# Performance work log

Measured on AMD Instinct MI355X. Metric: run time of the kernel, lower is better.

Reference implementation:

```python
import jax, jax.numpy as jnp
import numpy as np

B, L, D_LLM, C_OH, D = 256, 128, 1024, 64, 256
HEADS, LAYERS, EDGE_DIM, NET, E_PER = 4, 4, 64, 8, 256
N = B * L
DH = D // HEADS


def _layer_norm(x, g, b, eps=1e-5):
    m = x.mean(-1, keepdims=True)
    v = ((x - m) ** 2).mean(-1, keepdims=True)
    return (x - m) / jnp.sqrt(v + eps) * g + b


def _conv(h, src, dst, ea, Wq, bq, Wk, bk, Wv, bv, We, Ws, bs, Wb):
    # PyG TransformerConv (concat=True, beta=True, edge_dim): per-edge gather of Q(dst), K/V(src)
    q = (h @ Wq + bq)[dst].reshape(-1, HEADS, DH)
    k = (h @ Wk + bk)[src].reshape(-1, HEADS, DH)
    v = (h @ Wv + bv)[src].reshape(-1, HEADS, DH)
    e = (ea @ We).reshape(-1, HEADS, DH)
    k = k + e
    v = v + e
    alpha = (q * k).sum(-1) / jnp.sqrt(jnp.float32(DH))  # [E, H]
    amax = jax.ops.segment_max(alpha, dst, num_segments=N)  # segment softmax over dst
    ex = jnp.exp(alpha - amax[dst])
    den = jax.ops.segment_sum(ex, dst, num_segments=N)
    a = ex / den[dst]
    out = jax.ops.segment_sum(a[:, :, None] * v, dst, num_segments=N).reshape(N, D)
    xr = h @ Ws + bs  # root/skip projection
    beta = jax.nn.sigmoid(jnp.concatenate([out, xr, out - xr], axis=-1) @ Wb)  # [N,1]
    return beta * xr + (1.0 - beta) * out


def _gnorm(x, batch, w, b, ms, eps=1e-5):
    # PyG GraphNorm: per-graph mean with learnable mean_scale, per-graph variance
    cnt = jax.ops.segment_sum(jnp.ones((N,), x.dtype), batch, num_segments=B)[:, None]
    mean = jax.ops.segment_sum(x, batch, num_segments=B) / cnt
    out = x - mean[batch] * ms
    var = jax.ops.segment_sum(out * out, batch, num_segments=B) / cnt
    return w * out / jnp.sqrt(var + eps)[batch] + b


def _forward(atom_llm, atom_onehot, mask, edge_index, edge_type, batch,
             ln_llm_g, ln_llm_b, W_llm, b_llm, W_oh, edge_emb, edge_ln_g, edge_ln_b,
             Wq, bq, Wk, bk, Wv, bv, We, Ws, bs, Wb, gn_w, gn_b, gn_ms,
             W1, b1, W2, b2, out_ln_g, out_ln_b):
    x = (_layer_norm(atom_llm, ln_llm_g, ln_llm_b) @ W_llm + b_llm) + atom_onehot @ W_oh
    x = x * mask[..., None]
    h = x.reshape(N, D)  # all graphs full length L -> packing == reshape
    ea = _layer_norm(edge_emb[edge_type], edge_ln_g, edge_ln_b)
    src, dst = edge_index[0], edge_index[1]
    for l in range(LAYERS):
        h2 = _conv(h, src, dst, ea, Wq[l], bq[l], Wk[l], bk[l], Wv[l], bv[l], We[l], Ws[l], bs[l], Wb[l])
        h = _gnorm(h + h2, batch, gn_w[l], gn_b[l], gn_ms[l])
        h = jax.nn.gelu(h, approximate=False)
    ff = jax.nn.gelu(h @ W1 + b1, approximate=False) @ W2 + b2
    h = _layer_norm(h + ff, out_ln_g, out_ln_b)
    return h.reshape(B, L, D) * mask[..., None]


def setup_inputs():
    key = jax.random.key(0)
    ks = jax.random.split(key, 64)
    rng = np.random.default_rng(0)
    atom_llm = jax.random.normal(ks[0], (B, L, D_LLM), jnp.float32)
    atom_onehot = jax.random.uniform(ks[1], (B, L, C_OH), jnp.float32)
    mask = jnp.ones((B, L), jnp.float32)
    # per-graph random edges u != v, global offsets, undirected doubling
    u = rng.integers(0, L, size=(B, E_PER))
    v = (u + rng.integers(1, L, size=(B, E_PER))) % L
    et = rng.integers(0, NET, size=(B, E_PER)).reshape(-1)
    off = (np.arange(B) * L)[:, None]
    s = (u + off).reshape(-1)
    d = (v + off).reshape(-1)
    edge_index = jnp.asarray(np.stack([np.concatenate([s, d]), np.concatenate([d, s])]), jnp.int32)
    edge_type = jnp.asarray(np.concatenate([et, et]), jnp.int32)
    batch = jnp.repeat(jnp.arange(B, dtype=jnp.int32), L)

    def lin(k, i, o):
        s = 1.0 / np.sqrt(i)
        return jax.random.uniform(k, (i, o), jnp.float32, -s, s)

    st = lambda f, keys: jnp.stack([f(k) for k in keys])
    kq = jax.random.split(ks[10], LAYERS); kk = jax.random.split(ks[11], LAYERS)
    kv = jax.random.split(ks[12], LAYERS); ke = jax.random.split(ks[13], LAYERS)
    ksk = jax.random.split(ks[14], LAYERS); kb = jax.random.split(ks[15], LAYERS)
    return dict(
        atom_llm=atom_llm, atom_onehot=atom_onehot, mask=mask,
        edge_index=edge_index, edge_type=edge_type, batch=batch,
        ln_llm_g=jnp.ones((D_LLM,)), ln_llm_b=jnp.zeros((D_LLM,)),
        W_llm=lin(ks[2], D_LLM, D), b_llm=jnp.zeros((D,)),
        W_oh=lin(ks[3], C_OH, D),
        edge_emb=jax.random.normal(ks[4], (NET, EDGE_DIM), jnp.float32),
        edge_ln_g=jnp.ones((EDGE_DIM,)), edge_ln_b=jnp.zeros((EDGE_DIM,)),
        Wq=st(lambda k: lin(k, D, D), kq), bq=jnp.zeros((LAYERS, D)),
        Wk=st(lambda k: lin(k, D, D), kk), bk=jnp.zeros((LAYERS, D)),
        Wv=st(lambda k: lin(k, D, D), kv), bv=jnp.zeros((LAYERS, D)),
        We=st(lambda k: lin(k, EDGE_DIM, D), ke),
        Ws=st(lambda k: lin(k, D, D), ksk), bs=jnp.zeros((LAYERS, D)),
        Wb=st(lambda k: lin(k, 3 * D, 1), kb),
        gn_w=jnp.ones((LAYERS, D)), gn_b=jnp.zeros((LAYERS, D)), gn_ms=jnp.ones((LAYERS, D)),
        W1=lin(ks[6], D, 4 * D) * 0.5, b1=jnp.zeros((4 * D,)),
        W2=lin(ks[7], 4 * D, D) * 0.5, b2=jnp.zeros((D,)),
        out_ln_g=jnp.ones((D,)), out_ln_b=jnp.zeros((D,)),
    )


def reference(atom_llm, atom_onehot, mask, edge_index, edge_type, batch,
              ln_llm_g, ln_llm_b, W_llm, b_llm, W_oh, edge_emb, edge_ln_g, edge_ln_b,
              Wq, bq, Wk, bk, Wv, bv, We, Ws, bs, Wb, gn_w, gn_b, gn_ms,
              W1, b1, W2, b2, out_ln_g, out_ln_b):
    return _forward(atom_llm, atom_onehot, mask, edge_index, edge_type, batch,
                    ln_llm_g, ln_llm_b, W_llm, b_llm, W_oh, edge_emb, edge_ln_g, edge_ln_b,
                    Wq, bq, Wk, bk, Wv, bv, We, Ws, bs, Wb, gn_w, gn_b, gn_ms,
                    W1, b1, W2, b2, out_ln_g, out_ln_b)
```

## Files before the change

kernel.cpp:

```cpp
#include <hip/hip_runtime.h>
#include <math.h>

#define NB      256
#define LL      128
#define NN      32768
#define DLLM    1024
#define COH     64
#define DD      256
#define NLAYERS 4
#define EDIM    64
#define NETT    8
#define NE      131072

typedef unsigned short bf16_t;
typedef __bf16 bf16x8 __attribute__((ext_vector_type(8)));
typedef float f32x4v __attribute__((ext_vector_type(4)));

__device__ __forceinline__ float bf2f(bf16_t u){
    return __uint_as_float(((unsigned int)u) << 16);
}
__device__ __forceinline__ bf16_t f2bf(float f){
    unsigned int x = __float_as_uint(f);
    return (bf16_t)((x + 0x7fffu + ((x >> 16) & 1u)) >> 16);
}
__device__ __forceinline__ unsigned pack2(float a, float b){
    return (unsigned)f2bf(a) | ((unsigned)f2bf(b) << 16);
}
__device__ __forceinline__ float gelu_exact(float x){
    return 0.5f * x * (1.0f + erff(x * 0.70710678118654752440f));
}
__device__ __forceinline__ float wave_reduce_sum(float v){
#pragma unroll
    for (int off = 32; off; off >>= 1) v += __shfl_xor(v, off);
    return v;
}

__global__ void zero_kernel(int* __restrict__ p, int n){
    int i = blockIdx.x * blockDim.x + threadIdx.x;
    if (i < n) p[i] = 0;
}

__global__ __launch_bounds__(256)
void ln_concat_kernel(const float* __restrict__ A, const float* __restrict__ onehot,
                      const float* __restrict__ g, const float* __restrict__ b,
                      bf16_t* __restrict__ xln){
    int wave = threadIdx.x >> 6, lane = threadIdx.x & 63;
    int row = (blockIdx.x << 2) + wave;
    const float* p = A + (size_t)row * DLLM;
    float4 v[4];
    float s = 0.f, sq = 0.f;
#pragma unroll
    for (int c = 0; c < 4; c++){
        v[c] = *(const float4*)(p + c * 256 + (lane << 2));
        s  += v[c].x + v[c].y + v[c].z + v[c].w;
        sq += v[c].x*v[c].x + v[c].y*v[c].y + v[c].z*v[c].z + v[c].w*v[c].w;
    }
    s = wave_reduce_sum(s); sq = wave_reduce_sum(sq);
    float mean = s * (1.0f / DLLM);
    float var  = sq * (1.0f / DLLM) - mean * mean;
    float rstd = rsqrtf(var + 1e-5f);
    bf16_t* out = xln + (size_t)row * 1088;
#pragma unroll
    for (int c = 0; c < 4; c++){
        float4 g4 = *(const float4*)(g + c * 256 + (lane << 2));
        float4 b4 = *(const float4*)(b + c * 256 + (lane << 2));
        float rx = (v[c].x - mean) * rstd * g4.x + b4.x;
        float ry = (v[c].y - mean) * rstd * g4.y + b4.y;
        float rz = (v[c].z - mean) * rstd * g4.z + b4.z;
        float rw = (v[c].w - mean) * rstd * g4.w + b4.w;
        ushort4 u; u.x = f2bf(rx); u.y = f2bf(ry); u.z = f2bf(rz); u.w = f2bf(rw);
        *(ushort4*)(out + c * 256 + (lane << 2)) = u;
    }
    out[1024 + lane] = f2bf(onehot[(size_t)row * COH + lane]);
}

__global__ __launch_bounds__(256)
void edgeproj_kernel(const float* __restrict__ edge_emb,
                     const float* __restrict__ lg, const float* __restrict__ lb,
                     const float* __restrict__ We, float* __restrict__ eproj){
    int l = blockIdx.x >> 3, t = blockIdx.x & 7;
    __shared__ float ea[EDIM];
    int tid = threadIdx.x;
    if (tid < 64){
        float v = edge_emb[t * EDIM + tid];
        float s = v, sq = v * v;
#pragma unroll
        for (int off = 32; off; off >>= 1){ s += __shfl_xor(s, off); sq += __shfl_xor(sq, off); }
        float mean = s * (1.f/64.f);
        float var  = sq * (1.f/64.f) - mean * mean;
        float rstd = rsqrtf(var + 1e-5f);
        ea[tid] = (v - mean) * rstd * lg[tid] + lb[tid];
    }
    __syncthreads();
    const float* W = We + (size_t)l * EDIM * DD;
    float s = 0.f;
#pragma unroll
    for (int k = 0; k < EDIM; k++) s += ea[k] * W[k * DD + tid];
    eproj[((l << 3) + t) * DD + tid] = s;
}

__global__ void count_kernel(const int* __restrict__ dst, int* __restrict__ cnt){
    int e = blockIdx.x * blockDim.x + threadIdx.x;
    if (e < NE){
        int d = dst[e];
        if (d >= 0 && d < NN) atomicAdd(&cnt[d], 1);
    }
}

__global__ __launch_bounds__(1024)
void scan_kernel(const int* __restrict__ cnt, int* __restrict__ rowstart, int* __restrict__ cursor){
    __shared__ int sh[1024];
    int tid = threadIdx.x;
    int carry = 0;
    for (int base = 0; base < NN; base += 1024){
        int v = cnt[base + tid];
        sh[tid] = v; __syncthreads();
        for (int off = 1; off < 1024; off <<= 1){
            int t = (tid >= off) ? sh[tid - off] : 0;
            __syncthreads();
            sh[tid] += t;
            __syncthreads();
        }
        int excl = carry + sh[tid] - v;
        rowstart[base + tid] = excl;
        cursor[base + tid]   = excl;
        carry += sh[1023];
        __syncthreads();
    }
    if (tid == 0) rowstart[NN] = carry;
}

__global__ void scatter_kernel(const int* __restrict__ dst, int* __restrict__ cursor,
                               int* __restrict__ eidx){
    int e = blockIdx.x * blockDim.x + threadIdx.x;
    if (e < NE){
        int d = dst[e];
        if (d >= 0 && d < NN){
            int p = atomicAdd(&cursor[d], 1);
            if (p >= 0 && p < NE) eidx[p] = e;
        }
    }
}

__global__ void wcvt_in_kernel(const float* __restrict__ Wllm, const float* __restrict__ Woh,
                               bf16_t* __restrict__ dst){
    int idx = blockIdx.x * blockDim.x + threadIdx.x;
    if (idx >= 256 * 1088) return;
    int n = idx / 1088, k = idx % 1088;
    float v = (k < 1024) ? Wllm[(size_t)k * 256 + n] : Woh[(size_t)(k - 1024) * 256 + n];
    dst[idx] = f2bf(v);
}

__global__ void wcvt_qkvs_kernel(const float* __restrict__ Wq, const float* __restrict__ Wk,
                                 const float* __restrict__ Wv, const float* __restrict__ Ws,
                                 bf16_t* __restrict__ dst){
    int idx = blockIdx.x * blockDim.x + threadIdx.x;
    if (idx >= NLAYERS * 1024 * 256) return;
    int l = idx >> 18, rem = idx & 262143;
    int n = rem >> 8, k = rem & 255;
    int sel = n >> 8, nn = n & 255;
    const float* W = (sel == 0) ? Wq : (sel == 1) ? Wk : (sel == 2) ? Wv : Ws;
    dst[idx] = f2bf(W[(size_t)l * 65536 + (size_t)k * 256 + nn]);
}

__global__ void wcvt_w1_kernel(const float* __restrict__ W1, bf16_t* __restrict__ dst){
    int idx = blockIdx.x * blockDim.x + threadIdx.x;
    if (idx >= 1024 * 256) return;
    int n = idx >> 8, k = idx & 255;
    dst[idx] = f2bf(W1[(size_t)k * 1024 + n]);
}

__global__ void wcvt_w2_kernel(const float* __restrict__ W2, bf16_t* __restrict__ dst){
    int idx = blockIdx.x * blockDim.x + threadIdx.x;
    if (idx >= 256 * 1024) return;
    int n = idx >> 10, k = idx & 1023;
    dst[idx] = f2bf(W2[(size_t)k * 256 + n]);
}

__global__ void pack_bias_kernel(const float* __restrict__ bq, const float* __restrict__ bk,
                                 const float* __restrict__ bv, const float* __restrict__ bs,
                                 float* __restrict__ dst){
    int idx = blockIdx.x * blockDim.x + threadIdx.x;
    if (idx >= NLAYERS * 1024) return;
    int l = idx >> 10, n = idx & 1023;
    int sel = n >> 8, nn = n & 255;
    const float* B = (sel == 0) ? bq : (sel == 1) ? bk : (sel == 2) ? bv : bs;
    dst[idx] = B[l * 256 + nn];
}

template<bool A_F32, bool HAS_BIAS, bool GELU_EP, bool MASK_EP, bool WRITE_F32, bool WRITE_BF16>
__global__ __launch_bounds__(256)
void mfma_gemm(const void* __restrict__ Av, const bf16_t* __restrict__ BT,
               float* __restrict__ Cf, bf16_t* __restrict__ Cb,
               int Ncols, int K,
               const float* __restrict__ bias, const float* __restrict__ mask)
{
    __shared__ bf16_t As[128][40];
    __shared__ bf16_t Bs[128][40];
    const int tid  = threadIdx.x;
    const int rowBase = blockIdx.y << 7;
    const int colBase = blockIdx.x << 7;
    const int lane = tid & 63;
    const int wave = tid >> 6;
    const int wm = wave >> 1, wn = wave & 1;
    const int lhi = lane >> 4, llo = lane & 15;
    const int r0 = tid >> 2;
    const int q0 = (tid & 3) << 3;

    f32x4v acc[4][4];
#pragma unroll
    for (int m = 0; m < 4; m++)
#pragma unroll
        for (int n = 0; n < 4; n++)
            acc[m][n] = (f32x4v){0.f, 0.f, 0.f, 0.f};

    const int nk = K >> 5;
    for (int ks = 0; ks < nk; ks++){
        const int k0 = ks << 5;
        if constexpr (A_F32){
            const float* Ap = (const float*)Av;
#pragma unroll
            for (int half = 0; half < 2; half++){
                int r = r0 + half * 64;
                const float* p = Ap + (size_t)(rowBase + r) * K + (k0 + q0);
                float4 a = *(const float4*)p;
                float4 b = *(const float4*)(p + 4);
                uint4 pk;
                pk.x = pack2(a.x, a.y); pk.y = pack2(a.z, a.w);
                pk.z = pack2(b.x, b.y); pk.w = pack2(b.z, b.w);
                *(uint4*)&As[r][q0] = pk;
            }
        } else {
            const bf16_t* Ap = (const bf16_t*)Av;
#pragma unroll
            for (int half = 0; half < 2; half++){
                int r = r0 + half * 64;
                *(uint4*)&As[r][q0] = *(const uint4*)(Ap + (size_t)(rowBase + r) * K + (k0 + q0));
            }
        }
#pragma unroll
        for (int half = 0; half < 2; half++){
            int r = r0 + half * 64;
            *(uint4*)&Bs[r][q0] = *(const uint4*)(BT + (size_t)(colBase + r) * K + (k0 + q0));
        }
        __syncthreads();
        bf16x8 af[4], bfr[4];
#pragma unroll
        for (int m = 0; m < 4; m++)
            af[m] = *(const bf16x8*)&As[(wm << 6) + (m << 4) + llo][lhi << 3];
#pragma unroll
        for (int n = 0; n < 4; n++)
            bfr[n] = *(const bf16x8*)&Bs[(wn << 6) + (n << 4) + llo][lhi << 3];
#pragma unroll
        for (int m = 0; m < 4; m++)
#pragma unroll
            for (int n = 0; n < 4; n++)
                acc[m][n] = __builtin_amdgcn_mfma_f32_16x16x32_bf16(af[m], bfr[n], acc[m][n], 0, 0, 0);
        __syncthreads();
    }

#pragma unroll
    for (int m = 0; m < 4; m++){
        const int rowb = rowBase + (wm << 6) + (m << 4) + (lhi << 2);
#pragma unroll
        for (int n = 0; n < 4; n++){
            const int col = colBase + (wn << 6) + (n << 4) + llo;
            float bv = 0.f;
            if constexpr (HAS_BIAS) bv = bias[col];
#pragma unroll
            for (int r = 0; r < 4; r++){
                float v = acc[m][n][r] + bv;
                if constexpr (GELU_EP) v = gelu_exact(v);
                if constexpr (MASK_EP) v *= mask[rowb + r];
                if constexpr (WRITE_F32) Cf[(size_t)(rowb + r) * Ncols + col] = v;
                if constexpr (WRITE_BF16) Cb[(size_t)(rowb + r) * Ncols + col] = f2bf(v);
            }
        }
    }
}

__global__ __launch_bounds__(256)
void attn_beta_kernel(const bf16_t* __restrict__ QKVS, const float* __restrict__ h,
                      const int* __restrict__ rowstart, const int* __restrict__ eidx,
                      const int* __restrict__ src, const int* __restrict__ etype,
                      const float* __restrict__ eproj, const float* __restrict__ Wb,
                      float* __restrict__ S)
{
    int node = blockIdx.x;
    int wave = threadIdx.x >> 6, lane = threadIdx.x & 63;
    int fdim = (wave << 6) + lane;
    __shared__ float sh_a[4][256];
    __shared__ int   sh_e[256];
    __shared__ float sh_red[4];
    __shared__ float sh_beta;
    int s0 = rowstart[node];
    int deg = rowstart[node + 1] - s0;
    if (deg > 256) deg = 256;
    if (deg < 0) deg = 0;
    if (threadIdx.x < deg){
        int e = eidx[s0 + threadIdx.x];
        int sv = src[e]; if (sv < 0 || sv >= NN) sv = 0;
        sh_e[threadIdx.x] = (sv << 3) | (etype[e] & 7);
    }
    __syncthreads();
    float q = bf2f(QKVS[(size_t)node * 1024 + fdim]);
    float ep[NETT];
#pragma unroll
    for (int t = 0; t < NETT; t++) ep[t] = eproj[t * DD + fdim];
    float m = -1e30f;
    for (int i = 0; i < deg; i++){
        int pk = sh_e[i];
        int s = pk >> 3, t = pk & 7;
        float kv = bf2f(QKVS[(size_t)s * 1024 + 256 + fdim]) + ep[t];
        float d = q * kv;
#pragma unroll
        for (int off = 32; off; off >>= 1) d += __shfl_xor(d, off);
        d *= 0.125f;
        if (lane == 0) sh_a[wave][i] = d;
        m = fmaxf(m, d);
    }
    float den = 0.f;
    for (int i = 0; i < deg; i++){
        float ex = expf(sh_a[wave][i] - m);
        if (lane == 0) sh_a[wave][i] = ex;
        den += ex;
    }
    float invden = (deg > 0) ? 1.f / den : 0.f;
    float acc = 0.f;
    for (int i = 0; i < deg; i++){
        int pk = sh_e[i];
        int s = pk >> 3, t = pk & 7;
        float vv = bf2f(QKVS[(size_t)s * 1024 + 512 + fdim]) + ep[t];
        acc += sh_a[wave][i] * invden * vv;
    }
    float xr = bf2f(QKVS[(size_t)node * 1024 + 768 + fdim]);
    float part = acc * Wb[fdim] + xr * Wb[256 + fdim] + (acc - xr) * Wb[512 + fdim];
    part = wave_reduce_sum(part);
    if (lane == 0) sh_red[wave] = part;
    __syncthreads();
    if (threadIdx.x == 0){
        float p = sh_red[0] + sh_red[1] + sh_red[2] + sh_red[3];
        sh_beta = 1.f / (1.f + expf(-p));
    }
    __syncthreads();
    float beta = sh_beta;
    S[(size_t)node * DD + fdim] = h[(size_t)node * DD + fdim] + beta * xr + (1.f - beta) * acc;
}

__global__ __launch_bounds__(256)
void graphnorm_gelu_kernel(const float* __restrict__ xin, const float* __restrict__ w,
                           const float* __restrict__ b, const float* __restrict__ ms,
                           float* __restrict__ hout)
{
    int g = blockIdx.x, d = threadIdx.x;
    const float* base = xin + (size_t)g * LL * DD + d;
    float s = 0.f;
    for (int n = 0; n < LL; n++) s += base[n * DD];
    float sub = s * (1.f / LL) * ms[d];
    float var = 0.f;
    for (int n = 0; n < LL; n++){ float t = base[n * DD] - sub; var += t * t; }
    var *= (1.f / LL);
    float rs = rsqrtf(var + 1e-5f);
    float wd = w[d], bd = b[d];
    float* ob = hout + (size_t)g * LL * DD + d;
    for (int n = 0; n < LL; n++){
        float t = (base[n * DD] - sub) * rs * wd + bd;
        ob[n * DD] = gelu_exact(t);
    }
}

__global__ __launch_bounds__(256)
void final_ln_kernel(const float* __restrict__ h, const float* __restrict__ ff,
                     const float* __restrict__ g, const float* __restrict__ b,
                     const float* __restrict__ mask, float* __restrict__ outp)
{
    int wave = threadIdx.x >> 6, lane = threadIdx.x & 63;
    int node = (blockIdx.x << 2) + wave;
    int d0 = lane << 2;
    float4 hv = *(const float4*)(h  + (size_t)node * DD + d0);
    float4 fv = *(const float4*)(ff + (size_t)node * DD + d0);
    float4 v; v.x = hv.x + fv.x; v.y = hv.y + fv.y; v.z = hv.z + fv.z; v.w = hv.w + fv.w;
    float s  = v.x + v.y + v.z + v.w;
    float sq = v.x*v.x + v.y*v.y + v.z*v.z + v.w*v.w;
    s = wave_reduce_sum(s); sq = wave_reduce_sum(sq);
    float mean = s * (1.f / DD);
    float var  = sq * (1.f / DD) - mean * mean;
    float rs = rsqrtf(var + 1e-5f);
    float mk = mask[node];
    float4 g4 = *(const float4*)(g + d0), b4 = *(const float4*)(b + d0);
    float4 r;
    r.x = ((v.x - mean) * rs * g4.x + b4.x) * mk;
    r.y = ((v.y - mean) * rs * g4.y + b4.y) * mk;
    r.z = ((v.z - mean) * rs * g4.z + b4.z) * mk;
    r.w = ((v.w - mean) * rs * g4.w + b4.w) * mk;
    *(float4*)(outp + (size_t)node * DD + d0) = r;
}

extern "C" void kernel_launch(void* const* d_in, const int* in_sizes, int n_in,
                              void* d_out, int out_size, void* d_ws, size_t ws_size,
                              hipStream_t stream)
{
    if (n_in < 33) return;
    if (in_sizes[0] != NN * DLLM) return;
    if (in_sizes[3] != 2 * NE) return;
    if (in_sizes[8] != DLLM * DD) return;
    if (in_sizes[27] != DD * 4 * DD) return;
    if (out_size != NN * DD) return;

    const float* atom_llm    = (const float*)d_in[0];
    const float* atom_onehot = (const float*)d_in[1];
    const float* mask        = (const float*)d_in[2];
    const int*   edge_index  = (const int*)d_in[3];
    const int*   etype       = (const int*)d_in[4];
    const float* ln_llm_g    = (const float*)d_in[6];
    const float* ln_llm_b    = (const float*)d_in[7];
    const float* W_llm       = (const float*)d_in[8];
    const float* b_llm       = (const float*)d_in[9];
    const float* W_oh        = (const float*)d_in[10];
    const float* edge_emb    = (const float*)d_in[11];
    const float* edge_ln_g   = (const float*)d_in[12];
    const float* edge_ln_b   = (const float*)d_in[13];
    const float* Wq          = (const float*)d_in[14];
    const float* bq          = (const float*)d_in[15];
    const float* Wk          = (const float*)d_in[16];
    const float* bk          = (const float*)d_in[17];
    const float* Wv          = (const float*)d_in[18];
    const float* bv          = (const float*)d_in[19];
    const float* We          = (const float*)d_in[20];
    const float* Ws          = (const float*)d_in[21];
    const float* bs          = (const float*)d_in[22];
    const float* Wb          = (const float*)d_in[23];
    const float* gn_w        = (const float*)d_in[24];
    const float* gn_b        = (const float*)d_in[25];
    const float* gn_ms       = (const float*)d_in[26];
    const float* W1          = (const float*)d_in[27];
    const float* b1          = (const float*)d_in[28];
    const float* W2          = (const float*)d_in[29];
    const float* b2          = (const float*)d_in[30];
    const float* out_ln_g    = (const float*)d_in[31];
    const float* out_ln_b    = (const float*)d_in[32];

    const int* srcv = edge_index;
    const int* dstv = edge_index + NE;

    char* ws = (char*)d_ws;
    size_t off = 0;
    auto alloc = [&](size_t bytes) -> char* {
        char* p = ws + off; off += (bytes + 255) / 256 * 256; return p;
    };
    float*  h    = (float*)alloc((size_t)NN * DD * sizeof(float));
    bf16_t* reg3 = (bf16_t*)alloc((size_t)NN * 1088 * sizeof(bf16_t));
    bf16_t* wt_in   = (bf16_t*)alloc((size_t)256 * 1088 * sizeof(bf16_t));
    bf16_t* wt_qkvs = (bf16_t*)alloc((size_t)NLAYERS * 1024 * 256 * sizeof(bf16_t));
    bf16_t* wt_w1   = (bf16_t*)alloc((size_t)1024 * 256 * sizeof(bf16_t));
    bf16_t* wt_w2   = (bf16_t*)alloc((size_t)256 * 1024 * sizeof(bf16_t));
    float*  biasp   = (float*)alloc((size_t)NLAYERS * 1024 * sizeof(float));
    float*  eproj   = (float*)alloc((size_t)NLAYERS * NETT * DD * sizeof(float));
    int* cnt      = (int*)alloc((size_t)NN * sizeof(int));
    int* rowstart = (int*)alloc((size_t)(NN + 1) * sizeof(int));
    int* cursor   = (int*)alloc((size_t)NN * sizeof(int));
    int* eidx     = (int*)alloc((size_t)NE * sizeof(int));
    bf16_t* xln  = reg3;
    bf16_t* qkvs = reg3;
    bf16_t* t1   = reg3;
    float*  S    = (float*)d_out;

    if (ws_size < off) return;

    zero_kernel<<<NN / 256, 256, 0, stream>>>(cnt, NN);
    count_kernel<<<NE / 256, 256, 0, stream>>>(dstv, cnt);
    scan_kernel<<<1, 1024, 0, stream>>>(cnt, rowstart, cursor);
    scatter_kernel<<<NE / 256, 256, 0, stream>>>(dstv, cursor, eidx);

    ln_concat_kernel<<<NN / 4, 256, 0, stream>>>(atom_llm, atom_onehot, ln_llm_g, ln_llm_b, xln);
    edgeproj_kernel<<<NLAYERS * NETT, 256, 0, stream>>>(edge_emb, edge_ln_g, edge_ln_b, We, eproj);
    wcvt_in_kernel<<<(256 * 1088 + 255) / 256, 256, 0, stream>>>(W_llm, W_oh, wt_in);
    wcvt_qkvs_kernel<<<(NLAYERS * 1024 * 256) / 256, 256, 0, stream>>>(Wq, Wk, Wv, Ws, wt_qkvs);
    wcvt_w1_kernel<<<(1024 * 256) / 256, 256, 0, stream>>>(W1, wt_w1);
    wcvt_w2_kernel<<<(256 * 1024) / 256, 256, 0, stream>>>(W2, wt_w2);
    pack_bias_kernel<<<(NLAYERS * 1024) / 256, 256, 0, stream>>>(bq, bk, bv, bs, biasp);

    {
        dim3 grid(DD / 128, NN / 128);
        mfma_gemm<false, true, false, true, true, false><<<grid, 256, 0, stream>>>(
            xln, wt_in, h, nullptr, DD, 1088, b_llm, mask);
    }

    for (int l = 0; l < NLAYERS; l++){
        dim3 grid(1024 / 128, NN / 128);
        mfma_gemm<true, true, false, false, false, true><<<grid, 256, 0, stream>>>(
            h, wt_qkvs + (size_t)l * 1024 * 256, nullptr, qkvs, 1024, DD,
            biasp + (size_t)l * 1024, nullptr);

        attn_beta_kernel<<<NN, 256, 0, stream>>>(qkvs, h, rowstart, eidx, srcv, etype,
                                                 eproj + (size_t)l * NETT * DD,
                                                 Wb + (size_t)l * 768, S);

        graphnorm_gelu_kernel<<<NB, 256, 0, stream>>>(S, gn_w + l * DD, gn_b + l * DD,
                                                      gn_ms + l * DD, h);
    }

    {
        dim3 grid1(1024 / 128, NN / 128);
        mfma_gemm<true, true, true, false, false, true><<<grid1, 256, 0, stream>>>(
            h, wt_w1, nullptr, t1, 1024, DD, b1, nullptr);
        dim3 grid2(DD / 128, NN / 128);
        mfma_gemm<false, true, false, false, true, false><<<grid2, 256, 0, stream>>>(
            t1, wt_w2, S, nullptr, DD, 1024, b2, nullptr);
        final_ln_kernel<<<NN / 4, 256, 0, stream>>>(h, S, out_ln_g, out_ln_b, mask,
                                                    (float*)d_out);
    }
}
```

Before: 1.264 ms.

## Process attention per graph with K/V staged in LDS and online softmax

Replaces the one-block-per-node attention kernel with one 512-thread block per graph. Each block stages the graph's 128 K and V rows plus the edge projections in shared memory, and each wave handles 16 nodes. Each lane covers 4 features and uses a 16-lane reduction per head, and the softmax runs online in chunks. The scatter now stores the packed local source index and edge type, which removes the eidx/src/etype indirection. This assumes every edge's source lies in the same graph as its destination (src & 127); edges that cross graphs would be computed wrongly. Launching only 256 blocks with about 144KB of LDS each may also limit occupancy.

Result: faster. 1.130 ms (-10.6%).

```diff
diff --git a/kernel.cpp b/kernel.cpp
--- a/kernel.cpp
+++ b/kernel.cpp
@@ -11,6 +11,7 @@
 #define EDIM    64
 #define NETT    8
 #define NE      131072
+#define CHUNK   16
 
 typedef unsigned short bf16_t;
 typedef __bf16 bf16x8 __attribute__((ext_vector_type(8)));
@@ -130,14 +131,18 @@
     if (tid == 0) rowstart[NN] = carry;
 }
 
-__global__ void scatter_kernel(const int* __restrict__ dst, int* __restrict__ cursor,
-                               int* __restrict__ eidx){
+__global__ void scatter_kernel(const int* __restrict__ dst, const int* __restrict__ src,
+                               const int* __restrict__ etype, int* __restrict__ cursor,
+                               int* __restrict__ epack){
     int e = blockIdx.x * blockDim.x + threadIdx.x;
     if (e < NE){
         int d = dst[e];
         if (d >= 0 && d < NN){
             int p = atomicAdd(&cursor[d], 1);
-            if (p >= 0 && p < NE) eidx[p] = e;
+            if (p >= 0 && p < NE){
+                int sv = src[e]; if (sv < 0 || sv >= NN) sv = 0;
+                epack[p] = ((sv & 127) << 3) | (etype[e] & 7);
+            }
         }
     }
 }
@@ -279,72 +284,94 @@
     }
 }
 
-__global__ __launch_bounds__(256)
-void attn_beta_kernel(const bf16_t* __restrict__ QKVS, const float* __restrict__ h,
-                      const int* __restrict__ rowstart, const int* __restrict__ eidx,
-                      const int* __restrict__ src, const int* __restrict__ etype,
-                      const float* __restrict__ eproj, const float* __restrict__ Wb,
-                      float* __restrict__ S)
+__global__ __launch_bounds__(512)
+void attn_graph_kernel(const bf16_t* __restrict__ QKVS, const float* __restrict__ h,
+                       const int* __restrict__ rowstart, const int* __restrict__ epack,
+                       const float* __restrict__ eproj, const float* __restrict__ Wb,
+                       float* __restrict__ S)
 {
-    int node = blockIdx.x;
-    int wave = threadIdx.x >> 6, lane = threadIdx.x & 63;
-    int fdim = (wave << 6) + lane;
-    __shared__ float sh_a[4][256];
-    __shared__ int   sh_e[256];
-    __shared__ float sh_red[4];
-    __shared__ float sh_beta;
-    int s0 = rowstart[node];
-    int deg = rowstart[node + 1] - s0;
-    if (deg > 256) deg = 256;
-    if (deg < 0) deg = 0;
-    if (threadIdx.x < deg){
-        int e = eidx[s0 + threadIdx.x];
-        int sv = src[e]; if (sv < 0 || sv >= NN) sv = 0;
-        sh_e[threadIdx.x] = (sv << 3) | (etype[e] & 7);
-    }
+    __shared__ bf16_t Kl[128][256];
+    __shared__ bf16_t Vl[128][256];
+    __shared__ float  epl[8][256];
+    __shared__ float  al[8][CHUNK][4];
+    const int g = blockIdx.x;
+    const int tid = threadIdx.x;
+    const int wave = tid >> 6, lane = tid & 63;
+    const int hgrp = lane >> 4;
+    const int d4 = lane << 2;
+    const size_t gbase = (size_t)g * 128 * 1024;
+
+    for (int i = tid; i < 128 * 32; i += 512){
+        int n = i >> 5, c = (i & 31) << 3;
+        *(uint4*)&Kl[n][c] = *(const uint4*)(QKVS + gbase + (size_t)n * 1024 + 256 + c);
+        *(uint4*)&Vl[n][c] = *(const uint4*)(QKVS + gbase + (size_t)n * 1024 + 512 + c);
+    }
+    for (int i = tid; i < 8 * 256; i += 512) epl[i >> 8][i & 255] = eproj[i];
     __syncthreads();
-    float q = bf2f(QKVS[(size_t)node * 1024 + fdim]);
-    float ep[NETT];
-#pragma unroll
-    for (int t = 0; t < NETT; t++) ep[t] = eproj[t * DD + fdim];
-    float m = -1e30f;
-    for (int i = 0; i < deg; i++){
-        int pk = sh_e[i];
-        int s = pk >> 3, t = pk & 7;
-        float kv = bf2f(QKVS[(size_t)s * 1024 + 256 + fdim]) + ep[t];
-        float d = q * kv;
-#pragma unroll
-        for (int off = 32; off; off >>= 1) d += __shfl_xor(d, off);
-        d *= 0.125f;
-        if (lane == 0) sh_a[wave][i] = d;
-        m = fmaxf(m, d);
-    }
-    float den = 0.f;
-    for (int i = 0; i < deg; i++){
-        float ex = expf(sh_a[wave][i] - m);
-        if (lane == 0) sh_a[wave][i] = ex;
-        den += ex;
-    }
-    float invden = (deg > 0) ? 1.f / den : 0.f;
-    float acc = 0.f;
-    for (int i = 0; i < deg; i++){
-        int pk = sh_e[i];
-        int s = pk >> 3, t = pk & 7;
-        float vv = bf2f(QKVS[(size_t)s * 1024 + 512 + fdim]) + ep[t];
-        acc += sh_a[wave][i] * invden * vv;
-    }
-    float xr = bf2f(QKVS[(size_t)node * 1024 + 768 + fdim]);
-    float part = acc * Wb[fdim] + xr * Wb[256 + fdim] + (acc - xr) * Wb[512 + fdim];
-    part = wave_reduce_sum(part);
-    if (lane == 0) sh_red[wave] = part;
-    __syncthreads();
-    if (threadIdx.x == 0){
-        float p = sh_red[0] + sh_red[1] + sh_red[2] + sh_red[3];
-        sh_beta = 1.f / (1.f + expf(-p));
-    }
-    __syncthreads();
-    float beta = sh_beta;
-    S[(size_t)node * DD + fdim] = h[(size_t)node * DD + fdim] + beta * xr + (1.f - beta) * acc;
+
+    float4 w0 = *(const float4*)(Wb + d4);
+    float4 w1 = *(const float4*)(Wb + 256 + d4);
+    float4 w2 = *(const float4*)(Wb + 512 + d4);
+
+    for (int ni = 0; ni < 16; ni++){
+        int nl = (wave << 4) + ni;
+        int node = (g << 7) + nl;
+        int s0 = rowstart[node];
+        int deg = rowstart[node + 1] - s0;
+        if (deg < 0) deg = 0;
+        ushort4 qu = *(const ushort4*)(QKVS + gbase + (size_t)nl * 1024 + d4);
+        float q0 = bf2f(qu.x), q1 = bf2f(qu.y), q2 = bf2f(qu.z), q3 = bf2f(qu.w);
+        float m = -1e30f, den = 0.f;
+        float v0 = 0.f, v1 = 0.f, v2 = 0.f, v3 = 0.f;
+        for (int c0 = 0; c0 < deg; c0 += CHUNK){
+            int ce = deg - c0; if (ce > CHUNK) ce = CHUNK;
+            for (int i = 0; i < ce; i++){
+                int pk = epack[s0 + c0 + i];
+                int sl = pk >> 3, t = pk & 7;
+                ushort4 ku = *(const ushort4*)&Kl[sl][d4];
+                float4 ev = *(const float4*)&epl[t][d4];
+                float d = q0 * (bf2f(ku.x) + ev.x) + q1 * (bf2f(ku.y) + ev.y)
+                        + q2 * (bf2f(ku.z) + ev.z) + q3 * (bf2f(ku.w) + ev.w);
+                d += __shfl_xor(d, 1); d += __shfl_xor(d, 2);
+                d += __shfl_xor(d, 4); d += __shfl_xor(d, 8);
+                if ((lane & 15) == 0) al[wave][i][hgrp] = d * 0.125f;
+            }
+            float cm = -1e30f;
+            for (int i = 0; i < ce; i++) cm = fmaxf(cm, al[wave][i][hgrp]);
+            float mnew = fmaxf(m, cm);
+            float scale = expf(m - mnew);
+            den *= scale; v0 *= scale; v1 *= scale; v2 *= scale; v3 *= scale;
+            for (int i = 0; i < ce; i++){
+                int pk = epack[s0 + c0 + i];
+                int sl = pk >> 3, t = pk & 7;
+                float w = expf(al[wave][i][hgrp] - mnew);
+                den += w;
+                ushort4 vu = *(const ushort4*)&Vl[sl][d4];
+                float4 ev = *(const float4*)&epl[t][d4];
+                v0 = fmaf(w, bf2f(vu.x) + ev.x, v0);
+                v1 = fmaf(w, bf2f(vu.y) + ev.y, v1);
+                v2 = fmaf(w, bf2f(vu.z) + ev.z, v2);
+                v3 = fmaf(w, bf2f(vu.w) + ev.w, v3);
+            }
+            m = mnew;
+        }
+        float inv = (den > 0.f) ? 1.f / den : 0.f;
+        v0 *= inv; v1 *= inv; v2 *= inv; v3 *= inv;
+        ushort4 xu = *(const ushort4*)(QKVS + gbase + (size_t)nl * 1024 + 768 + d4);
+        float x0 = bf2f(xu.x), x1 = bf2f(xu.y), x2 = bf2f(xu.z), x3 = bf2f(xu.w);
+        float part = v0*w0.x + v1*w0.y + v2*w0.z + v3*w0.w
+                   + x0*w1.x + x1*w1.y + x2*w1.z + x3*w1.w
+                   + (v0-x0)*w2.x + (v1-x1)*w2.y + (v2-x2)*w2.z + (v3-x3)*w2.w;
+        part = wave_reduce_sum(part);
+        float beta = 1.f / (1.f + expf(-part));
+        float4 hv = *(const float4*)(h + ((size_t)node << 8) + d4);
+        float4 r;
+        r.x = hv.x + beta * x0 + (1.f - beta) * v0;
+        r.y = hv.y + beta * x1 + (1.f - beta) * v1;
+        r.z = hv.z + beta * x2 + (1.f - beta) * v2;
+        r.w = hv.w + beta * x3 + (1.f - beta) * v3;
+        *(float4*)(S + ((size_t)node << 8) + d4) = r;
+    }
 }
 
 __global__ __launch_bounds__(256)
@@ -459,7 +486,7 @@
     int* cnt      = (int*)alloc((size_t)NN * sizeof(int));
     int* rowstart = (int*)alloc((size_t)(NN + 1) * sizeof(int));
     int* cursor   = (int*)alloc((size_t)NN * sizeof(int));
-    int* eidx     = (int*)alloc((size_t)NE * sizeof(int));
+    int* epack    = (int*)alloc((size_t)NE * sizeof(int));
     bf16_t* xln  = reg3;
     bf16_t* qkvs = reg3;
     bf16_t* t1   = reg3;
@@ -470,7 +497,7 @@
     zero_kernel<<<NN / 256, 256, 0, stream>>>(cnt, NN);
     count_kernel<<<NE / 256, 256, 0, stream>>>(dstv, cnt);
     scan_kernel<<<1, 1024, 0, stream>>>(cnt, rowstart, cursor);
-    scatter_kernel<<<NE / 256, 256, 0, stream>>>(dstv, cursor, eidx);
+    scatter_kernel<<<NE / 256, 256, 0, stream>>>(dstv, srcv, etype, cursor, epack);
 
     ln_concat_kernel<<<NN / 4, 256, 0, stream>>>(atom_llm, atom_onehot, ln_llm_g, ln_llm_b, xln);
     edgeproj_kernel<<<NLAYERS * NETT, 256, 0, stream>>>(edge_emb, edge_ln_g, edge_ln_b, We, eproj);
@@ -492,9 +519,9 @@
             h, wt_qkvs + (size_t)l * 1024 * 256, nullptr, qkvs, 1024, DD,
             biasp + (size_t)l * 1024, nullptr);
 
-        attn_beta_kernel<<<NN, 256, 0, stream>>>(qkvs, h, rowstart, eidx, srcv, etype,
-                                                 eproj + (size_t)l * NETT * DD,
-                                                 Wb + (size_t)l * 768, S);
+        attn_graph_kernel<<<NB, 512, 0, stream>>>(qkvs, h, rowstart, epack,
+                                                  eproj + (size_t)l * NETT * DD,
+                                                  Wb + (size_t)l * 768, S);
 
         graphnorm_gelu_kernel<<<NB, 256, 0, stream>>>(S, gn_w + l * DD, gn_b + l * DD,
                                                       gn_ms + l * DD, h);
```
